# Kernel optimization log

Hardware: AMD Instinct MI355X
Metric: run time of the kernel (lower is better)

## Reference

```python
import jax, jax.numpy as jnp
import numpy as np

K = 3        # kernel_size
UM = 2       # um_dim
EPS = 1e-6
SLOPE = 0.01 # F.leaky_relu default negative slope


def setup_inputs() -> dict:
    key = jax.random.key(0)
    k1, k2, k3 = jax.random.split(key, 3)
    B, C, H, Wd = 16, 64, 64, 64
    O = 64
    xx = jax.random.normal(k1, (B, C, H, Wd), dtype=jnp.float32)
    W = jax.random.normal(k2, (O, C, K, K), dtype=jnp.float32) * 0.05
    b = jax.random.normal(k3, (O,), dtype=jnp.float32) * 0.05
    return {"xx": xx, "W": W, "b": b}


def reference(xx, W, b):
    B, C, H, Wd = xx.shape
    O = W.shape[0]
    p = (K - 1) // 2
    # replicate pad (mode='replicate' in torch == 'edge' in numpy/jax)
    xp = jnp.pad(xx, ((0, 0), (0, 0), (p, p), (p, p)), mode='edge')
    # unfold -> patches[b, c, i, j, h, w] = xp[b, c, h+i, w+j]; stride==1
    pats = jnp.stack(
        [xp[:, :, i:i + H, j:j + Wd] for i in range(K) for j in range(K)],
        axis=2,
    ).reshape(B, C, K, K, H, Wd)
    # min-max "std" normalization over (channel-group, ki, kj)
    g = pats.reshape(B, C // UM, UM, K, K, H, Wd)
    stds = (g.max(axis=(1, 3, 4), keepdims=True)
            - g.min(axis=(1, 3, 4), keepdims=True))  # [B,1,UM,1,1,H,W]
    normed = (g / (stds + EPS)).reshape(B, C, K, K, H, Wd)
    # patch-conv with stride=k on the unfolded image is equivalent to this
    # per-position contraction; big[b,c,h*k+j, w*k+i] = normed[b,c,i,j,h,w]
    # so the kernel indexes as W[o, c, j, i].
    out = jnp.einsum('bcijhw,ocji->bohw', normed, W) + b[None, :, None, None]
    out = jnp.where(out >= 0, out, SLOPE * out)  # leaky_relu
    # inverse transform: re-scale by (stds + eps)
    stds_s = stds.reshape(B, 1, UM, H, Wd)
    out = out.reshape(B, O // UM, UM, H, Wd) * (stds_s + EPS)
    return out.reshape(B, O, H, Wd)
```

## Files before the change

### kernel.cpp

```cpp
#include <hip/hip_runtime.h>
#include <hip/hip_bf16.h>

#define B_  16
#define C_  64
#define H_  64
#define W_  64
#define O_  64
#define EPS 1e-6f
#define SLOPE 0.01f

typedef __bf16  bf16x8 __attribute__((ext_vector_type(8)));
typedef float   f32x4  __attribute__((ext_vector_type(4)));

#define XT_WS_OFF  131072
#define PMM_WS_OFF 16908288

__device__ __forceinline__ unsigned short f2bf(float f) {
  unsigned u = __float_as_uint(f);
  u += 0x7fffu + ((u >> 16) & 1u);
  return (unsigned short)(u >> 16);
}

__device__ __forceinline__ int clampi(int v, int lo, int hi) {
  return v < lo ? lo : (v > hi ? hi : v);
}

__global__ void wtransform_kernel(const float* __restrict__ Wsrc,
                                  unsigned short* __restrict__ Wt) {
  int idx = blockIdx.x * 256 + threadIdx.x;
  if (idx >= O_ * C_ * 9) return;
  int i = idx % 3;
  int j = (idx / 3) % 3;
  int c = (idx / 9) % C_;
  int o = idx / (9 * C_);
  int tap = i * 3 + j;
  Wt[((tap * 2 + (c & 1)) * 64 + o) * 32 + (c >> 1)] = f2bf(Wsrc[idx]);
}

__global__ __launch_bounds__(256)
void prep_kernel(const float* __restrict__ x,
                 char* __restrict__ xt,
                 float* __restrict__ pmm) {
  __shared__ float red[2][2][4][64];
  const int bb = blockIdx.x;
  const int b  = bb >> 6;
  const int h  = bb & 63;
  const int qq = threadIdx.x >> 6;
  const int w  = threadIdx.x & 63;

  const float* xp = x + (((size_t)b * C_ + qq * 16) * H_ + h) * W_ + w;
  float f[16];
  #pragma unroll
  for (int k = 0; k < 16; ++k) f[k] = xp[(size_t)k * (H_ * W_)];

  float mn[2] = {3.4e38f, 3.4e38f}, mx[2] = {-3.4e38f, -3.4e38f};
  unsigned pk[2][4];
  #pragma unroll
  for (int k = 0; k < 16; ++k) {
    const int p = k & 1, e = k >> 1;
    mn[p] = fminf(mn[p], f[k]);
    mx[p] = fmaxf(mx[p], f[k]);
    const unsigned h16 = f2bf(f[k]);
    if (e & 1) pk[p][e >> 1] |= (h16 << 16);
    else       pk[p][e >> 1]  = h16;
  }
  #pragma unroll
  for (int p = 0; p < 2; ++p)
    *(uint4*)(xt + ((size_t)(((b * 2 + p) * 4 + qq) * 4096) + h * 64 + w) * 16) =
        make_uint4(pk[p][0], pk[p][1], pk[p][2], pk[p][3]);

  red[0][0][qq][w] = mn[0];
  red[0][1][qq][w] = mn[1];
  red[1][0][qq][w] = mx[0];
  red[1][1][qq][w] = mx[1];
  __syncthreads();

  const int map = threadIdx.x >> 7;
  const int p   = (threadIdx.x >> 6) & 1;
  const int w2  = threadIdx.x & 63;
  float v;
  if (map == 0)
    v = fminf(fminf(red[0][p][0][w2], red[0][p][1][w2]),
              fminf(red[0][p][2][w2], red[0][p][3][w2]));
  else
    v = fmaxf(fmaxf(red[1][p][0][w2], red[1][p][1][w2]),
              fmaxf(red[1][p][2][w2], red[1][p][3][w2]));
  pmm[((size_t)(map * 16 + b) * 2 + p) * 4096 + h * 64 + w2] = v;
}

__global__ __launch_bounds__(256, 4)
void gemm_kernel(const char* __restrict__ xt,
                 const unsigned short* __restrict__ Wt,
                 const float* __restrict__ pmm,
                 const float* __restrict__ bias,
                 float* __restrict__ out) {
  const int bb   = blockIdx.x;
  const int b    = bb >> 6;
  const int h    = bb & 63;
  const int wv   = threadIdx.x >> 6;
  const int lane = threadIdx.x & 63;
  const int l15  = lane & 15;
  const int q    = lane >> 4;
  const int o0   = wv * 16;

  float si[2], se[2];
  #pragma unroll
  for (int p = 0; p < 2; ++p) {
    float mn = 3.4e38f, mx = -3.4e38f;
    #pragma unroll
    for (int r = 0; r < 3; ++r) {
      const int hr = clampi(h - 1 + r, 0, H_ - 1);
      mn = fminf(mn, pmm[((size_t)(0 * 16 + b) * 2 + p) * 4096 + hr * 64 + lane]);
      mx = fmaxf(mx, pmm[((size_t)(1 * 16 + b) * 2 + p) * 4096 + hr * 64 + lane]);
    }
    const float mnl = __shfl(mn, clampi(lane - 1, 0, 63));
    const float mnr = __shfl(mn, clampi(lane + 1, 0, 63));
    const float mxl = __shfl(mx, clampi(lane - 1, 0, 63));
    const float mxr = __shfl(mx, clampi(lane + 1, 0, 63));
    mn = fminf(mn, fminf(mnl, mnr));
    mx = fmaxf(mx, fmaxf(mxl, mxr));
    const float sv = (mx - mn) + EPS;
    se[p] = sv;
    si[p] = 1.0f / sv;
  }

  const f32x4 zero = {0.0f, 0.0f, 0.0f, 0.0f};
  f32x4 oacc[4];
  #pragma unroll
  for (int nt = 0; nt < 4; ++nt) oacc[nt] = zero;

  #pragma unroll 1
  for (int p = 0; p < 2; ++p) {
    bf16x8 af[9];
    #pragma unroll
    for (int t9 = 0; t9 < 9; ++t9)
      af[t9] = *(const bf16x8*)(Wt + ((t9 * 2 + p) * 64 + o0 + l15) * 32 + q * 8);

    const char* plane = xt + (size_t)(((b * 2 + p) * 4 + q) * 4096) * 16;
    f32x4 acc[4];
    #pragma unroll
    for (int nt = 0; nt < 4; ++nt) acc[nt] = zero;

    #pragma unroll
    for (int i = 0; i < 3; ++i) {
      const int hr = clampi(h - 1 + i, 0, H_ - 1);
      const char* row = plane + (size_t)hr * 64 * 16;
      #pragma unroll
      for (int nt = 0; nt < 4; ++nt) {
        bf16x8 bfr[3];
        #pragma unroll
        for (int j = 0; j < 3; ++j) {
          const int wc = clampi(nt * 16 + l15 + j - 1, 0, W_ - 1);
          bfr[j] = *(const bf16x8*)(row + wc * 16);
        }
        #pragma unroll
        for (int j = 0; j < 3; ++j)
          acc[nt] = __builtin_amdgcn_mfma_f32_16x16x32_bf16(
              af[i * 3 + j], bfr[j], acc[nt], 0, 0, 0);
      }
    }

    #pragma unroll
    for (int nt = 0; nt < 4; ++nt) {
      const float sv = __shfl(si[p], nt * 16 + l15);
      #pragma unroll
      for (int reg = 0; reg < 4; ++reg)
        oacc[nt][reg] += acc[nt][reg] * sv;
    }
  }

  float bv[4];
  #pragma unroll
  for (int reg = 0; reg < 4; ++reg) bv[reg] = bias[o0 + q * 4 + reg];

  #pragma unroll
  for (int nt = 0; nt < 4; ++nt) {
    const int wpx = nt * 16 + l15;
    const float se0 = __shfl(se[0], wpx);
    const float se1 = __shfl(se[1], wpx);
    #pragma unroll
    for (int reg = 0; reg < 4; ++reg) {
      const int o = o0 + q * 4 + reg;
      float v = oacc[nt][reg] + bv[reg];
      v = v >= 0.0f ? v : SLOPE * v;
      v *= (reg & 1) ? se1 : se0;
      out[(((size_t)b * O_ + o) * H_ + h) * W_ + wpx] = v;
    }
  }
}

extern "C" void kernel_launch(void* const* d_in, const int* in_sizes, int n_in,
                              void* d_out, int out_size, void* d_ws, size_t ws_size,
                              hipStream_t stream) {
  const float* x    = (const float*)d_in[0];
  const float* Wsrc = (const float*)d_in[1];
  const float* bias = (const float*)d_in[2];
  float* out = (float*)d_out;

  unsigned short* Wt = (unsigned short*)d_ws;
  char*  xt  = (char*)d_ws + XT_WS_OFF;
  float* pmm = (float*)((char*)d_ws + PMM_WS_OFF);

  wtransform_kernel<<<144, 256, 0, stream>>>(Wsrc, Wt);
  prep_kernel<<<1024, 256, 0, stream>>>(x, xt, pmm);
  gemm_kernel<<<1024, 256, 0, stream>>>(xt, Wt, pmm, bias, out);
}
```

Baseline: 92.82 us.

## Fuse weight transform into prep, coalesce input loads via LDS, repack bf16 layout

```diff
diff --git a/kernel.cpp b/kernel.cpp
--- a/kernel.cpp
+++ b/kernel.cpp
@@ -13,7 +13,9 @@
 typedef float   f32x4  __attribute__((ext_vector_type(4)));
 
 #define XT_WS_OFF  131072
-#define PMM_WS_OFF 16908288
+#define PMM_WS_OFF 8519680
+
+#define RAWC 65
 
 __device__ __forceinline__ unsigned short f2bf(float f) {
   unsigned u = __float_as_uint(f);
@@ -25,67 +27,91 @@
   return v < lo ? lo : (v > hi ? hi : v);
 }
 
-__global__ void wtransform_kernel(const float* __restrict__ Wsrc,
-                                  unsigned short* __restrict__ Wt) {
-  int idx = blockIdx.x * 256 + threadIdx.x;
-  if (idx >= O_ * C_ * 9) return;
-  int i = idx % 3;
-  int j = (idx / 3) % 3;
-  int c = (idx / 9) % C_;
-  int o = idx / (9 * C_);
-  int tap = i * 3 + j;
-  Wt[((tap * 2 + (c & 1)) * 64 + o) * 32 + (c >> 1)] = f2bf(Wsrc[idx]);
-}
-
 __global__ __launch_bounds__(256)
 void prep_kernel(const float* __restrict__ x,
+                 const float* __restrict__ Wsrc,
+                 unsigned short* __restrict__ Wt,
                  char* __restrict__ xt,
                  float* __restrict__ pmm) {
-  __shared__ float red[2][2][4][64];
-  const int bb = blockIdx.x;
-  const int b  = bb >> 6;
-  const int h  = bb & 63;
-  const int qq = threadIdx.x >> 6;
-  const int w  = threadIdx.x & 63;
-
-  const float* xp = x + (((size_t)b * C_ + qq * 16) * H_ + h) * W_ + w;
-  float f[16];
-  #pragma unroll
-  for (int k = 0; k < 16; ++k) f[k] = xp[(size_t)k * (H_ * W_)];
-
-  float mn[2] = {3.4e38f, 3.4e38f}, mx[2] = {-3.4e38f, -3.4e38f};
-  unsigned pk[2][4];
-  #pragma unroll
-  for (int k = 0; k < 16; ++k) {
-    const int p = k & 1, e = k >> 1;
-    mn[p] = fminf(mn[p], f[k]);
-    mx[p] = fmaxf(mx[p], f[k]);
-    const unsigned h16 = f2bf(f[k]);
-    if (e & 1) pk[p][e >> 1] |= (h16 << 16);
-    else       pk[p][e >> 1]  = h16;
-  }
-  #pragma unroll
-  for (int p = 0; p < 2; ++p)
-    *(uint4*)(xt + ((size_t)(((b * 2 + p) * 4 + qq) * 4096) + h * 64 + w) * 16) =
-        make_uint4(pk[p][0], pk[p][1], pk[p][2], pk[p][3]);
-
-  red[0][0][qq][w] = mn[0];
-  red[0][1][qq][w] = mn[1];
-  red[1][0][qq][w] = mx[0];
-  red[1][1][qq][w] = mx[1];
+  __shared__ float raw[64 * RAWC];
+  __shared__ float red[2][4][64];
+
+  if (blockIdx.x >= 1024) {
+    const int idx0 = (int)(blockIdx.x - 1024) * 4096 + threadIdx.x * 16;
+    const float4* src = (const float4*)(Wsrc + idx0);
+    float f[16];
+    #pragma unroll
+    for (int k = 0; k < 4; ++k) {
+      const float4 v = src[k];
+      f[k * 4 + 0] = v.x; f[k * 4 + 1] = v.y;
+      f[k * 4 + 2] = v.z; f[k * 4 + 3] = v.w;
+    }
+    #pragma unroll
+    for (int e = 0; e < 16; ++e) {
+      const int idx = idx0 + e;
+      const int i = idx % 3;
+      const int j = (idx / 3) % 3;
+      const int c = (idx / 9) & 63;
+      const int o = idx / 576;
+      const int tap = i * 3 + j;
+      Wt[((tap * 2 + (c & 1)) * 64 + o) * 32 + (c >> 1)] = f2bf(f[e]);
+    }
+    return;
+  }
+
+  const int b    = blockIdx.x >> 6;
+  const int h    = blockIdx.x & 63;
+  const int lane = threadIdx.x & 63;
+  const int wv   = threadIdx.x >> 6;
+
+  {
+    const int w4 = (lane & 15) * 4;
+    const int cb = wv * 16 + (lane >> 4);
+    #pragma unroll
+    for (int k = 0; k < 4; ++k) {
+      const int c = cb + k * 4;
+      const float4 v = *(const float4*)(x + (((size_t)b * C_ + c) * H_ + h) * W_ + w4);
+      raw[(w4 + 0) * RAWC + c] = v.x;
+      raw[(w4 + 1) * RAWC + c] = v.y;
+      raw[(w4 + 2) * RAWC + c] = v.z;
+      raw[(w4 + 3) * RAWC + c] = v.w;
+    }
+  }
   __syncthreads();
 
-  const int map = threadIdx.x >> 7;
-  const int p   = (threadIdx.x >> 6) & 1;
-  const int w2  = threadIdx.x & 63;
-  float v;
-  if (map == 0)
-    v = fminf(fminf(red[0][p][0][w2], red[0][p][1][w2]),
-              fminf(red[0][p][2][w2], red[0][p][3][w2]));
-  else
-    v = fmaxf(fmaxf(red[1][p][0][w2], red[1][p][1][w2]),
-              fmaxf(red[1][p][2][w2], red[1][p][3][w2]));
-  pmm[((size_t)(map * 16 + b) * 2 + p) * 4096 + h * 64 + w2] = v;
+  {
+    const int w    = threadIdx.x & 63;
+    const int half = threadIdx.x >> 6;
+    const int p    = half & 1;
+    const int c2s  = half >> 1;
+    float mn = 3.4e38f, mx = -3.4e38f;
+    unsigned pk[8];
+    #pragma unroll
+    for (int u = 0; u < 16; ++u) {
+      const int c2 = c2s * 16 + u;
+      const float f = raw[w * RAWC + 2 * c2 + p];
+      mn = fminf(mn, f);
+      mx = fmaxf(mx, f);
+      const unsigned hb = f2bf(f);
+      if (u & 1) pk[u >> 1] |= (hb << 16);
+      else       pk[u >> 1]  = hb;
+    }
+    char* dst = xt + ((size_t)(((b * 64 + h) * 2 + p) * 64 + w)) * 64 + c2s * 32;
+    *(uint4*)(dst)      = make_uint4(pk[0], pk[1], pk[2], pk[3]);
+    *(uint4*)(dst + 16) = make_uint4(pk[4], pk[5], pk[6], pk[7]);
+    red[0][half][w] = mn;
+    red[1][half][w] = mx;
+  }
+  __syncthreads();
+
+  {
+    const int map = threadIdx.x >> 7;
+    const int p   = (threadIdx.x >> 6) & 1;
+    const int w   = threadIdx.x & 63;
+    const float a = red[map][p][w], c = red[map][2 + p][w];
+    const float v = map ? fmaxf(a, c) : fminf(a, c);
+    pmm[((size_t)(map * 16 + b) * 2 + p) * 4096 + h * 64 + w] = v;
+  }
 }
 
 __global__ __launch_bounds__(256, 4)
@@ -94,9 +120,8 @@
                  const float* __restrict__ pmm,
                  const float* __restrict__ bias,
                  float* __restrict__ out) {
-  const int bb   = blockIdx.x;
-  const int b    = bb >> 6;
-  const int h    = bb & 63;
+  const int b    = blockIdx.x >> 6;
+  const int h    = blockIdx.x & 63;
   const int wv   = threadIdx.x >> 6;
   const int lane = threadIdx.x & 63;
   const int l15  = lane & 15;
@@ -136,7 +161,6 @@
     for (int t9 = 0; t9 < 9; ++t9)
       af[t9] = *(const bf16x8*)(Wt + ((t9 * 2 + p) * 64 + o0 + l15) * 32 + q * 8);
 
-    const char* plane = xt + (size_t)(((b * 2 + p) * 4 + q) * 4096) * 16;
     f32x4 acc[4];
     #pragma unroll
     for (int nt = 0; nt < 4; ++nt) acc[nt] = zero;
@@ -144,14 +168,14 @@
     #pragma unroll
     for (int i = 0; i < 3; ++i) {
       const int hr = clampi(h - 1 + i, 0, H_ - 1);
-      const char* row = plane + (size_t)hr * 64 * 16;
+      const char* row = xt + ((size_t)((b * 64 + hr) * 2 + p)) * 4096;
       #pragma unroll
       for (int nt = 0; nt < 4; ++nt) {
         bf16x8 bfr[3];
         #pragma unroll
         for (int j = 0; j < 3; ++j) {
           const int wc = clampi(nt * 16 + l15 + j - 1, 0, W_ - 1);
-          bfr[j] = *(const bf16x8*)(row + wc * 16);
+          bfr[j] = *(const bf16x8*)(row + wc * 64 + q * 16);
         }
         #pragma unroll
         for (int j = 0; j < 3; ++j)
@@ -201,7 +225,6 @@
   char*  xt  = (char*)d_ws + XT_WS_OFF;
   float* pmm = (float*)((char*)d_ws + PMM_WS_OFF);
 
-  wtransform_kernel<<<144, 256, 0, stream>>>(Wsrc, Wt);
-  prep_kernel<<<1024, 256, 0, stream>>>(x, xt, pmm);
+  prep_kernel<<<1024 + 9, 256, 0, stream>>>(x, Wsrc, Wt, xt, pmm);
   gemm_kernel<<<1024, 256, 0, stream>>>(xt, Wt, pmm, bias, out);
 }
```

New measurement: 100.1 us. 1.08x slower.
